# Optimization experiments

Measured on AMD Instinct MI355X. Metric: run time of the kernel, lower is better.

The kernel has to match this reference:

```python
import jax, jax.numpy as jnp
import numpy as np

N_NODES = 100000
N_EDGES = 1000000
NUM_GRAPHS = 500
EPS = 1e-5


def gcn_conv(x, src, dst, W, b, n_nodes):
    # PyG GCNConv: h = x @ W, symmetric norm with self-loops, aggregate at dst, add bias
    h = x @ W
    deg = jnp.zeros((n_nodes,), h.dtype).at[dst].add(1.0) + 1.0  # in-degree + self-loop
    dis = jax.lax.rsqrt(deg)
    msg = h[src] * (dis[src] * dis[dst])[:, None]               # [E, F] gather
    agg = jnp.zeros_like(h).at[dst].add(msg)                    # scatter-add
    return agg + h * (dis * dis)[:, None] + b                   # self-loop term + bias


def bn_eval(x, g, be, m, v):
    return (x - m) * jax.lax.rsqrt(v + EPS) * g + be


def setup_inputs() -> dict:
    key = jax.random.key(0)
    ks = jax.random.split(key, 8)
    edge_index = jax.random.randint(ks[0], (2, N_EDGES), 0, N_NODES, dtype=jnp.int32)
    batch = jnp.sort(jax.random.randint(ks[1], (N_NODES,), 0, NUM_GRAPHS, dtype=jnp.int32))
    d_in, h1, h2, hc, nc = 64, 64, 32, 16, 2
    return {
        "x": jax.random.normal(ks[2], (N_NODES, d_in), jnp.float32),
        "edge_index": edge_index,
        "batch": batch,
        "W1": jax.random.normal(ks[3], (d_in, h1), jnp.float32) / np.sqrt(d_in),
        "b1": jnp.zeros((h1,), jnp.float32),
        "g1": jnp.ones((h1,), jnp.float32),
        "be1": jnp.zeros((h1,), jnp.float32),
        "m1": jnp.zeros((h1,), jnp.float32),
        "v1": jnp.ones((h1,), jnp.float32),
        "W2": jax.random.normal(ks[4], (h1, h2), jnp.float32) / np.sqrt(h1),
        "b2": jnp.zeros((h2,), jnp.float32),
        "g2": jnp.ones((h2,), jnp.float32),
        "be2": jnp.zeros((h2,), jnp.float32),
        "m2": jnp.zeros((h2,), jnp.float32),
        "v2": jnp.ones((h2,), jnp.float32),
        "Wc1": jax.random.normal(ks[5], (h2, hc), jnp.float32) / np.sqrt(h2),
        "bc1": jnp.zeros((hc,), jnp.float32),
        "Wc2": jax.random.normal(ks[6], (hc, nc), jnp.float32) / np.sqrt(hc),
        "bc2": jnp.zeros((nc,), jnp.float32),
    }


def reference(x, edge_index, batch, W1, b1, g1, be1, m1, v1,
              W2, b2, g2, be2, m2, v2, Wc1, bc1, Wc2, bc2):
    src, dst = edge_index[0], edge_index[1]
    n = x.shape[0]
    # encoder layer 1: GCNConv -> BN(eval) -> ReLU  (dropout off in eval)
    h = jax.nn.relu(bn_eval(gcn_conv(x, src, dst, W1, b1, n), g1, be1, m1, v1))
    # encoder layer 2
    h = jax.nn.relu(bn_eval(gcn_conv(h, src, dst, W2, b2, n), g2, be2, m2, v2))
    # global mean pool over graphs
    sums = jax.ops.segment_sum(h, batch, num_segments=NUM_GRAPHS)
    cnts = jax.ops.segment_sum(jnp.ones((n,), h.dtype), batch, num_segments=NUM_GRAPHS)
    z = sums / jnp.maximum(cnts, 1.0)[:, None]                  # [NUM_GRAPHS, h2]
    # classifier MLP
    return jax.nn.relu(z @ Wc1 + bc1) @ Wc2 + bc2               # [NUM_GRAPHS, num_classes]
```

## Files before the change

kernel.cpp:

```cpp
#include <hip/hip_runtime.h>
#include <hip/hip_bf16.h>


#define CHUNK 4096

typedef float floatx2 __attribute__((ext_vector_type(2)));

__global__ void k_zero_misc(int* __restrict__ bucketCnt, float* __restrict__ sums,
                            int nSums) {
    int i = blockIdx.x * blockDim.x + threadIdx.x;
    if (i < 512) bucketCnt[i] = 0;
    int j = i - 512;
    if (j >= 0 && j < nSums) sums[j] = 0.f;
}

__global__ __launch_bounds__(256) void k_hist(const int* __restrict__ dst,
                                              int* __restrict__ bucketCnt, int E) {
    __shared__ int lh[512];
    for (int i = threadIdx.x; i < 512; i += 256) lh[i] = 0;
    __syncthreads();
    int base = blockIdx.x * CHUNK;
    for (int i = threadIdx.x; i < CHUNK; i += 256) {
        int e = base + i;
        if (e < E) atomicAdd(&lh[dst[e] >> 8], 1);
    }
    __syncthreads();
    for (int i = threadIdx.x; i < 512; i += 256)
        if (lh[i]) atomicAdd(&bucketCnt[i], lh[i]);
}

__global__ void k_scan512(const int* __restrict__ bucketCnt,
                          int* __restrict__ bucketStart,
                          int* __restrict__ bucketCursor) {
    __shared__ int s[512];
    int tid = threadIdx.x;
    int v = bucketCnt[tid];
    s[tid] = v;
    __syncthreads();
    for (int off = 1; off < 512; off <<= 1) {
        int t = (tid >= off) ? s[tid - off] : 0;
        __syncthreads();
        s[tid] += t;
        __syncthreads();
    }
    int excl = s[tid] - v;
    bucketStart[tid] = excl;
    bucketCursor[tid] = excl;
    if (tid == 511) bucketStart[512] = s[511];
}

__global__ __launch_bounds__(256) void k_binpairs(
    const int* __restrict__ src, const int* __restrict__ dst,
    int* __restrict__ bucketCursor, unsigned* __restrict__ pairs, int E) {
    __shared__ int lh[512];
    __shared__ int lbase[512];
    for (int i = threadIdx.x; i < 512; i += 256) lh[i] = 0;
    __syncthreads();
    int base = blockIdx.x * CHUNK;
    for (int i = threadIdx.x; i < CHUNK; i += 256) {
        int e = base + i;
        if (e < E) atomicAdd(&lh[dst[e] >> 8], 1);
    }
    __syncthreads();
    for (int i = threadIdx.x; i < 512; i += 256) {
        int c = lh[i];
        lbase[i] = c ? atomicAdd(&bucketCursor[i], c) : 0;
        lh[i] = 0;
    }
    __syncthreads();
    for (int i = threadIdx.x; i < CHUNK; i += 256) {
        int e = base + i;
        if (e < E) {
            int d = dst[e];
            int b = d >> 8;
            int r = atomicAdd(&lh[b], 1);
            pairs[lbase[b] + r] = ((unsigned)src[e] << 8) | (unsigned)(d & 255);
        }
    }
}

__global__ __launch_bounds__(256) void k_csr(
    const unsigned* __restrict__ pairs, const int* __restrict__ bucketStart,
    int* __restrict__ rowStart, float* __restrict__ dis, int* __restrict__ perm,
    int n, int E) {
    __shared__ int cnt[256];
    __shared__ int s[256];
    __shared__ int cur[256];
    int b = blockIdx.x, tid = threadIdx.x;
    int r0 = bucketStart[b], r1 = bucketStart[b + 1];
    cnt[tid] = 0;
    __syncthreads();
    for (int i = r0 + tid; i < r1; i += 256) atomicAdd(&cnt[pairs[i] & 255], 1);
    __syncthreads();
    int v = cnt[tid];
    s[tid] = v;
    __syncthreads();
    for (int off = 1; off < 256; off <<= 1) {
        int t = (tid >= off) ? s[tid - off] : 0;
        __syncthreads();
        s[tid] += t;
        __syncthreads();
    }
    int excl = s[tid] - v;
    int node = b * 256 + tid;
    if (node < n) {
        rowStart[node] = r0 + excl;
        dis[node] = rsqrtf((float)v + 1.0f);
    }
    if (b == 0 && tid == 0) rowStart[n] = E;
    cur[tid] = excl;
    __syncthreads();
    for (int i = r0 + tid; i < r1; i += 256) {
        unsigned p = pairs[i];
        int lo = p & 255;
        int slot = atomicAdd(&cur[lo], 1);
        perm[r0 + slot] = (int)(p >> 8);
    }
}

__global__ __launch_bounds__(256) void k_gemm64(
    const float* __restrict__ x, const float* __restrict__ W,
    const float* __restrict__ dis, unsigned char* __restrict__ hs8, int n) {
    __shared__ float Ws[64 * 64];
    __shared__ float xs[128][65];
    const int tid = threadIdx.x;
    for (int i = tid * 4; i < 4096; i += 1024)
        *(float4*)&Ws[i] = *(const float4*)&W[i];
    const int base = blockIdx.x * 128;
    for (int i = tid; i < 2048; i += 256) {
        int r = i >> 4;
        int k = (i & 15) * 4;
        int row = base + r;
        float4 xv = (row < n) ? *(const float4*)&x[(size_t)row * 64 + k]
                              : make_float4(0.f, 0.f, 0.f, 0.f);
        xs[r][k] = xv.x; xs[r][k + 1] = xv.y; xs[r][k + 2] = xv.z; xs[r][k + 3] = xv.w;
    }
    __syncthreads();
    const int cg = tid & 7;
    const int rg = tid >> 3;
    float acc[4][8] = {};
#pragma unroll 4
    for (int k = 0; k < 64; ++k) {
        float w8[8];
        *(float4*)&w8[0] = *(const float4*)&Ws[k * 64 + cg * 8];
        *(float4*)&w8[4] = *(const float4*)&Ws[k * 64 + cg * 8 + 4];
        float x4[4];
#pragma unroll
        for (int rr = 0; rr < 4; ++rr) x4[rr] = xs[rg * 4 + rr][k];
#pragma unroll
        for (int rr = 0; rr < 4; ++rr)
#pragma unroll
            for (int cc = 0; cc < 8; ++cc)
                acc[rr][cc] = fmaf(x4[rr], w8[cc], acc[rr][cc]);
    }
#pragma unroll
    for (int rr = 0; rr < 4; ++rr) {
        int row = base + rg * 4 + rr;
        if (row >= n) break;
        float d = dis[row];
        float v0 = acc[rr][0] * d, v1 = acc[rr][1] * d;
        float v2 = acc[rr][2] * d, v3 = acc[rr][3] * d;
        float v4 = acc[rr][4] * d, v5 = acc[rr][5] * d;
        float v6 = acc[rr][6] * d, v7 = acc[rr][7] * d;
        int q0 = __builtin_amdgcn_cvt_pk_fp8_f32(v0, v1, 0, false);
        q0 = __builtin_amdgcn_cvt_pk_fp8_f32(v2, v3, q0, true);
        int q1 = __builtin_amdgcn_cvt_pk_fp8_f32(v4, v5, 0, false);
        q1 = __builtin_amdgcn_cvt_pk_fp8_f32(v6, v7, q1, true);
        uint2 q = {(unsigned)q0, (unsigned)q1};
        *(uint2*)&hs8[(size_t)row * 64 + cg * 8] = q;
    }
}

__global__ __launch_bounds__(256) void k_gather64f8_gemm32(
    const unsigned char* __restrict__ hs8, const int* __restrict__ rowStart,
    const int* __restrict__ perm, const float* __restrict__ dis,
    const float* __restrict__ b, const float* __restrict__ g,
    const float* __restrict__ be, const float* __restrict__ m,
    const float* __restrict__ v, const float* __restrict__ W2,
    unsigned char* __restrict__ hs2f8, int n) {
    __shared__ float W2s[64 * 32];
    __shared__ float actS[16][68];
    for (int i = threadIdx.x * 4; i < 2048; i += 1024)
        *(float4*)&W2s[i] = *(const float4*)&W2[i];
    __syncthreads();

    const unsigned* hsu = (const unsigned*)hs8;
    int c = threadIdx.x & 15;
    int ln = threadIdx.x >> 4;
    int node = (blockIdx.x * 256 + threadIdx.x) >> 4;
    if (node >= n) return;
    int r0 = rowStart[node], r1 = rowStart[node + 1];
    float d = dis[node];
    float a0, a1, a2, a3;
    {
        unsigned su = hsu[(size_t)node * 16 + c];
        floatx2 lo = __builtin_amdgcn_cvt_pk_f32_fp8(su, false);
        floatx2 hi = __builtin_amdgcn_cvt_pk_f32_fp8(su, true);
        a0 = lo[0]; a1 = lo[1]; a2 = hi[0]; a3 = hi[1];
    }
    int e = r0;
    for (; e + 7 < r1; e += 8) {
        int s0 = perm[e],     s1 = perm[e + 1], s2 = perm[e + 2], s3 = perm[e + 3];
        int s4 = perm[e + 4], s5 = perm[e + 5], s6 = perm[e + 6], s7 = perm[e + 7];
        unsigned u0 = hsu[(size_t)s0 * 16 + c];
        unsigned u1 = hsu[(size_t)s1 * 16 + c];
        unsigned u2 = hsu[(size_t)s2 * 16 + c];
        unsigned u3 = hsu[(size_t)s3 * 16 + c];
        unsigned u4 = hsu[(size_t)s4 * 16 + c];
        unsigned u5 = hsu[(size_t)s5 * 16 + c];
        unsigned u6 = hsu[(size_t)s6 * 16 + c];
        unsigned u7 = hsu[(size_t)s7 * 16 + c];
#pragma unroll
        for (int j = 0; j < 8; ++j) {
            unsigned u = j == 0 ? u0 : j == 1 ? u1 : j == 2 ? u2 : j == 3 ? u3
                       : j == 4 ? u4 : j == 5 ? u5 : j == 6 ? u6 : u7;
            floatx2 lo = __builtin_amdgcn_cvt_pk_f32_fp8(u, false);
            floatx2 hi = __builtin_amdgcn_cvt_pk_f32_fp8(u, true);
            a0 += lo[0]; a1 += lo[1]; a2 += hi[0]; a3 += hi[1];
        }
    }
    for (; e < r1; ++e) {
        unsigned u = hsu[(size_t)perm[e] * 16 + c];
        floatx2 lo = __builtin_amdgcn_cvt_pk_f32_fp8(u, false);
        floatx2 hi = __builtin_amdgcn_cvt_pk_f32_fp8(u, true);
        a0 += lo[0]; a1 += lo[1]; a2 += hi[0]; a3 += hi[1];
    }
    int f = 4 * c;
    float4 gv = *(const float4*)&g[f];
    float4 vv = *(const float4*)&v[f];
    float4 bv = *(const float4*)&b[f];
    float4 mv = *(const float4*)&m[f];
    float4 bev = *(const float4*)&be[f];
    float sc0 = gv.x * rsqrtf(vv.x + 1e-5f), sc1 = gv.y * rsqrtf(vv.y + 1e-5f);
    float sc2 = gv.z * rsqrtf(vv.z + 1e-5f), sc3 = gv.w * rsqrtf(vv.w + 1e-5f);
    float y0 = fmaf(a0 * d, sc0, (bv.x - mv.x) * sc0 + bev.x);
    float y1 = fmaf(a1 * d, sc1, (bv.y - mv.y) * sc1 + bev.y);
    float y2 = fmaf(a2 * d, sc2, (bv.z - mv.z) * sc2 + bev.z);
    float y3 = fmaf(a3 * d, sc3, (bv.w - mv.w) * sc3 + bev.w);
    float4 yv = {y0 > 0.f ? y0 : 0.f, y1 > 0.f ? y1 : 0.f,
                 y2 > 0.f ? y2 : 0.f, y3 > 0.f ? y3 : 0.f};
    *(float4*)&actS[ln][f] = yv;

    float o0 = 0.f, o1 = 0.f;
#pragma unroll
    for (int k = 0; k < 64; ++k) {
        float a = actS[ln][k];
        o0 = fmaf(a, W2s[k * 32 + 2 * c], o0);
        o1 = fmaf(a, W2s[k * 32 + 2 * c + 1], o1);
    }
    int q = __builtin_amdgcn_cvt_pk_fp8_f32(o0 * d, o1 * d, 0, false);
    *(unsigned short*)&hs2f8[(size_t)node * 32 + 2 * c] = (unsigned short)q;
}

__global__ __launch_bounds__(256) void k_gather32f8(
    const unsigned char* __restrict__ hs8, const int* __restrict__ rowStart,
    const int* __restrict__ perm, const float* __restrict__ dis,
    const float* __restrict__ b, const float* __restrict__ g,
    const float* __restrict__ be, const float* __restrict__ m,
    const float* __restrict__ v, float* __restrict__ act, int n) {
    const unsigned* hsu = (const unsigned*)hs8;
    int c = threadIdx.x & 7;
    int node = (blockIdx.x * 256 + threadIdx.x) >> 3;
    if (node >= n) return;
    int r0 = rowStart[node], r1 = rowStart[node + 1];
    float d = dis[node];
    float a0, a1, a2, a3;
    {
        unsigned su = hsu[(size_t)node * 8 + c];
        floatx2 lo = __builtin_amdgcn_cvt_pk_f32_fp8(su, false);
        floatx2 hi = __builtin_amdgcn_cvt_pk_f32_fp8(su, true);
        a0 = lo[0]; a1 = lo[1]; a2 = hi[0]; a3 = hi[1];
    }
    int e = r0;
    for (; e + 7 < r1; e += 8) {
        int s0 = perm[e],     s1 = perm[e + 1], s2 = perm[e + 2], s3 = perm[e + 3];
        int s4 = perm[e + 4], s5 = perm[e + 5], s6 = perm[e + 6], s7 = perm[e + 7];
        unsigned u0 = hsu[(size_t)s0 * 8 + c];
        unsigned u1 = hsu[(size_t)s1 * 8 + c];
        unsigned u2 = hsu[(size_t)s2 * 8 + c];
        unsigned u3 = hsu[(size_t)s3 * 8 + c];
        unsigned u4 = hsu[(size_t)s4 * 8 + c];
        unsigned u5 = hsu[(size_t)s5 * 8 + c];
        unsigned u6 = hsu[(size_t)s6 * 8 + c];
        unsigned u7 = hsu[(size_t)s7 * 8 + c];
#pragma unroll
        for (int j = 0; j < 8; ++j) {
            unsigned u = j == 0 ? u0 : j == 1 ? u1 : j == 2 ? u2 : j == 3 ? u3
                       : j == 4 ? u4 : j == 5 ? u5 : j == 6 ? u6 : u7;
            floatx2 lo = __builtin_amdgcn_cvt_pk_f32_fp8(u, false);
            floatx2 hi = __builtin_amdgcn_cvt_pk_f32_fp8(u, true);
            a0 += lo[0]; a1 += lo[1]; a2 += hi[0]; a3 += hi[1];
        }
    }
    for (; e < r1; ++e) {
        unsigned u = hsu[(size_t)perm[e] * 8 + c];
        floatx2 lo = __builtin_amdgcn_cvt_pk_f32_fp8(u, false);
        floatx2 hi = __builtin_amdgcn_cvt_pk_f32_fp8(u, true);
        a0 += lo[0]; a1 += lo[1]; a2 += hi[0]; a3 += hi[1];
    }
    int f = 4 * c;
    float4 gv = *(const float4*)&g[f];
    float4 vv = *(const float4*)&v[f];
    float4 bv = *(const float4*)&b[f];
    float4 mv = *(const float4*)&m[f];
    float4 bev = *(const float4*)&be[f];
    float sc0 = gv.x * rsqrtf(vv.x + 1e-5f), sc1 = gv.y * rsqrtf(vv.y + 1e-5f);
    float sc2 = gv.z * rsqrtf(vv.z + 1e-5f), sc3 = gv.w * rsqrtf(vv.w + 1e-5f);
    float y0 = fmaf(a0 * d, sc0, (bv.x - mv.x) * sc0 + bev.x);
    float y1 = fmaf(a1 * d, sc1, (bv.y - mv.y) * sc1 + bev.y);
    float y2 = fmaf(a2 * d, sc2, (bv.z - mv.z) * sc2 + bev.z);
    float y3 = fmaf(a3 * d, sc3, (bv.w - mv.w) * sc3 + bev.w);
    float4 o = {y0 > 0.f ? y0 : 0.f, y1 > 0.f ? y1 : 0.f,
                y2 > 0.f ? y2 : 0.f, y3 > 0.f ? y3 : 0.f};
    *(float4*)&act[(size_t)node * 32 + f] = o;
}

__global__ __launch_bounds__(256) void k_pool(
    const float* __restrict__ act2, const int* __restrict__ batch,
    float* __restrict__ sums, float* __restrict__ cnt, int n) {
    int f = threadIdx.x & 31;
    int chunk = (blockIdx.x * blockDim.x + threadIdx.x) >> 5;
    int nchunks = (gridDim.x * blockDim.x) >> 5;
    int per = (n + nchunks - 1) / nchunks;
    int i0 = chunk * per;
    int i1 = min(n, i0 + per);
    if (i0 >= n) return;
    float acc = 0.f, c = 0.f;
    int cur = batch[i0];
    for (int i = i0; i < i1; ++i) {
        int bg = batch[i];
        if (bg != cur) {
            atomicAdd(&sums[(size_t)cur * 32 + f], acc);
            if (f == 0) atomicAdd(&cnt[cur], c);
            acc = 0.f; c = 0.f; cur = bg;
        }
        acc += act2[(size_t)i * 32 + f];
        c += 1.f;
    }
    atomicAdd(&sums[(size_t)cur * 32 + f], acc);
    if (f == 0) atomicAdd(&cnt[cur], c);
}

__global__ void k_mlp(const float* __restrict__ sums, const float* __restrict__ cnt,
                      const float* __restrict__ Wc1, const float* __restrict__ bc1,
                      const float* __restrict__ Wc2, const float* __restrict__ bc2,
                      float* __restrict__ out, int G) {
    int g = blockIdx.x * blockDim.x + threadIdx.x;
    if (g >= G) return;
    float c = cnt[g];
    c = c < 1.f ? 1.f : c;
    float inv = 1.f / c;
    float z[32];
#pragma unroll
    for (int j = 0; j < 32; ++j) z[j] = sums[(size_t)g * 32 + j] * inv;
    float o0 = bc2[0], o1 = bc2[1];
#pragma unroll
    for (int k = 0; k < 16; ++k) {
        float t = bc1[k];
#pragma unroll
        for (int j = 0; j < 32; ++j) t = fmaf(z[j], Wc1[j * 16 + k], t);
        t = t > 0.f ? t : 0.f;
        o0 = fmaf(t, Wc2[k * 2 + 0], o0);
        o1 = fmaf(t, Wc2[k * 2 + 1], o1);
    }
    out[g * 2 + 0] = o0;
    out[g * 2 + 1] = o1;
}

extern "C" void kernel_launch(void* const* d_in, const int* in_sizes, int n_in,
                              void* d_out, int out_size, void* d_ws, size_t ws_size,
                              hipStream_t stream) {
    const float* x   = (const float*)d_in[0];
    const int* ei    = (const int*)d_in[1];
    const int* batch = (const int*)d_in[2];
    const float* W1  = (const float*)d_in[3];
    const float* b1  = (const float*)d_in[4];
    const float* g1  = (const float*)d_in[5];
    const float* be1 = (const float*)d_in[6];
    const float* m1  = (const float*)d_in[7];
    const float* v1  = (const float*)d_in[8];
    const float* W2  = (const float*)d_in[9];
    const float* b2  = (const float*)d_in[10];
    const float* g2  = (const float*)d_in[11];
    const float* be2 = (const float*)d_in[12];
    const float* m2  = (const float*)d_in[13];
    const float* v2  = (const float*)d_in[14];
    const float* Wc1 = (const float*)d_in[15];
    const float* bc1 = (const float*)d_in[16];
    const float* Wc2 = (const float*)d_in[17];
    const float* bc2 = (const float*)d_in[18];

    const int n = in_sizes[2];
    const int E = in_sizes[1] / 2;
    const int G = out_size / 2;
    const int* srcI = ei;
    const int* dstI = ei + E;
    const int NB = (n + 255) >> 8;

    char* p = (char*)d_ws;
    auto alloc = [&](size_t bytes) {
        char* r = p;
        p += (bytes + 255) & ~(size_t)255;
        return r;
    };
    float*    dis          = (float*)alloc((size_t)n * 4);
    int*      bucketCnt    = (int*)alloc(512 * 4);
    int*      bucketStart  = (int*)alloc(513 * 4);
    int*      bucketCursor = (int*)alloc(512 * 4);
    unsigned* pairs        = (unsigned*)alloc((size_t)E * 4);
    int*      perm         = (int*)alloc((size_t)E * 4);
    int*      rowStart     = (int*)alloc(((size_t)n + 1) * 4);
    unsigned char* hs1f8   = (unsigned char*)alloc((size_t)64 * n);
    unsigned char* hs2f8   = (unsigned char*)alloc((size_t)32 * n);
    float*    act2         = (float*)alloc((size_t)32 * n * 4);
    float*    sums         = (float*)alloc((size_t)32 * G * 4 + (size_t)G * 4);
    float*    cntG         = sums + (size_t)32 * G;

    const int NT = 256;
    const int nbE = (E + CHUNK - 1) / CHUNK;
    const int nSums = G * 33;

    k_zero_misc<<<(512 + nSums + NT - 1) / NT, NT, 0, stream>>>(bucketCnt, sums, nSums);
    k_hist<<<nbE, NT, 0, stream>>>(dstI, bucketCnt, E);
    k_scan512<<<1, 512, 0, stream>>>(bucketCnt, bucketStart, bucketCursor);
    k_binpairs<<<nbE, NT, 0, stream>>>(srcI, dstI, bucketCursor, pairs, E);
    k_csr<<<NB, NT, 0, stream>>>(pairs, bucketStart, rowStart, dis, perm, n, E);

    k_gemm64<<<(n + 127) / 128, NT, 0, stream>>>(x, W1, dis, hs1f8, n);
    k_gather64f8_gemm32<<<(n * 16 + NT - 1) / NT, NT, 0, stream>>>(
        hs1f8, rowStart, perm, dis, b1, g1, be1, m1, v1, W2, hs2f8, n);

    k_gather32f8<<<(n * 8 + NT - 1) / NT, NT, 0, stream>>>(hs2f8, rowStart, perm, dis,
                                                           b2, g2, be2, m2, v2, act2, n);
    k_pool<<<1024, NT, 0, stream>>>(act2, batch, sums, cntG, n);

    k_mlp<<<(G + NT - 1) / NT, NT, 0, stream>>>(sums, cntG, Wc1, bc1, Wc2, bc2,
                                                (float*)d_out, G);
}
```

Before: 150.0 us.

## Fuse all stages into one persistent cooperative kernel with grid-wide syncs

Replaces the chain of ten kernel launches with one persistent cooperative kernel of 1024 blocks. Each stage runs as a grid-stride loop and stages are separated by grid.sync(), which removes per-launch overhead and tail gaps between launches. The cost is that every phase is limited to the co-resident grid, and the GEMM now reads W1 from global memory with 32-row tiles instead of a shared-memory-staged 128-row tile. It also adds serialized single-thread scans and grid barriers, and falls back to the old multi-kernel path if occupancy is too low.

```diff
diff --git a/kernel.cpp b/kernel.cpp
--- a/kernel.cpp
+++ b/kernel.cpp
@@ -1,10 +1,391 @@
 #include <hip/hip_runtime.h>
 #include <hip/hip_bf16.h>
+#include <hip/hip_cooperative_groups.h>
+
+namespace cg = cooperative_groups;
 
 
 #define CHUNK 4096
 
 typedef float floatx2 __attribute__((ext_vector_type(2)));
+
+struct Params {
+    const float* x; const int* src; const int* dst; const int* batch;
+    const float* W1; const float* b1; const float* g1; const float* be1;
+    const float* m1; const float* v1;
+    const float* W2; const float* b2; const float* g2; const float* be2;
+    const float* m2; const float* v2;
+    const float* Wc1; const float* bc1; const float* Wc2; const float* bc2;
+    float* out;
+    float* dis; int* bucketCnt; int* bucketStart; int* bucketCursor;
+    unsigned* pairs; int* perm; int* rowStart;
+    unsigned char* hs1f8; unsigned char* hs2f8; float* act2;
+    float* sums; float* cntG;
+    int n, E, G, NB;
+};
+
+union SMem {
+    struct { int lh[512]; int lbase[512]; } hist;
+    struct { int s[512]; } scan;
+    struct { int cnt[256]; int s[256]; int cur[256]; } csr;
+    struct { float xs[32][65]; } gemm;
+    struct { float W2s[64 * 32]; float actS[16][68]; } fg;
+};
+
+__global__ __launch_bounds__(256, 4) void k_mono(Params p) {
+    cg::grid_group grid = cg::this_grid();
+    __shared__ SMem sm;
+    const int tid = threadIdx.x;
+    const int bid = blockIdx.x;
+    const int nBlk = gridDim.x;
+
+    for (int i = bid * 256 + tid; i < 512 + p.G * 33; i += nBlk * 256) {
+        if (i < 512) p.bucketCnt[i] = 0;
+        else p.sums[i - 512] = 0.f;
+    }
+    grid.sync();
+
+    for (int cb = bid; cb * CHUNK < p.E; cb += nBlk) {
+        for (int i = tid; i < 512; i += 256) sm.hist.lh[i] = 0;
+        __syncthreads();
+        int base = cb * CHUNK;
+        for (int i = tid; i < CHUNK; i += 256) {
+            int e = base + i;
+            if (e < p.E) atomicAdd(&sm.hist.lh[p.dst[e] >> 8], 1);
+        }
+        __syncthreads();
+        for (int i = tid; i < 512; i += 256)
+            if (sm.hist.lh[i]) atomicAdd(&p.bucketCnt[i], sm.hist.lh[i]);
+        __syncthreads();
+    }
+    grid.sync();
+
+    if (bid == 0) {
+        for (int i = tid; i < 512; i += 256) sm.scan.s[i] = p.bucketCnt[i];
+        __syncthreads();
+        if (tid == 0) {
+            int acc = 0;
+            for (int i = 0; i < 512; ++i) {
+                int v = sm.scan.s[i];
+                sm.scan.s[i] = acc;
+                acc += v;
+            }
+        }
+        __syncthreads();
+        for (int i = tid; i < 512; i += 256) {
+            int e = sm.scan.s[i];
+            p.bucketStart[i] = e;
+            p.bucketCursor[i] = e;
+        }
+        if (tid == 0) p.bucketStart[512] = p.E;
+    }
+    grid.sync();
+
+    for (int cb = bid; cb * CHUNK < p.E; cb += nBlk) {
+        for (int i = tid; i < 512; i += 256) sm.hist.lh[i] = 0;
+        __syncthreads();
+        int base = cb * CHUNK;
+        for (int i = tid; i < CHUNK; i += 256) {
+            int e = base + i;
+            if (e < p.E) atomicAdd(&sm.hist.lh[p.dst[e] >> 8], 1);
+        }
+        __syncthreads();
+        for (int i = tid; i < 512; i += 256) {
+            int c = sm.hist.lh[i];
+            sm.hist.lbase[i] = c ? atomicAdd(&p.bucketCursor[i], c) : 0;
+            sm.hist.lh[i] = 0;
+        }
+        __syncthreads();
+        for (int i = tid; i < CHUNK; i += 256) {
+            int e = base + i;
+            if (e < p.E) {
+                int d = p.dst[e];
+                int b = d >> 8;
+                int r = atomicAdd(&sm.hist.lh[b], 1);
+                p.pairs[sm.hist.lbase[b] + r] =
+                    ((unsigned)p.src[e] << 8) | (unsigned)(d & 255);
+            }
+        }
+        __syncthreads();
+    }
+    grid.sync();
+
+    for (int b = bid; b < p.NB; b += nBlk) {
+        int r0 = p.bucketStart[b], r1 = p.bucketStart[b + 1];
+        sm.csr.cnt[tid] = 0;
+        __syncthreads();
+        for (int i = r0 + tid; i < r1; i += 256)
+            atomicAdd(&sm.csr.cnt[p.pairs[i] & 255], 1);
+        __syncthreads();
+        int v = sm.csr.cnt[tid];
+        sm.csr.s[tid] = v;
+        __syncthreads();
+        for (int off = 1; off < 256; off <<= 1) {
+            int t = (tid >= off) ? sm.csr.s[tid - off] : 0;
+            __syncthreads();
+            sm.csr.s[tid] += t;
+            __syncthreads();
+        }
+        int excl = sm.csr.s[tid] - v;
+        int node = b * 256 + tid;
+        if (node < p.n) {
+            p.rowStart[node] = r0 + excl;
+            p.dis[node] = rsqrtf((float)v + 1.0f);
+        }
+        if (b == 0 && tid == 0) p.rowStart[p.n] = p.E;
+        sm.csr.cur[tid] = excl;
+        __syncthreads();
+        for (int i = r0 + tid; i < r1; i += 256) {
+            unsigned pr = p.pairs[i];
+            int lo = pr & 255;
+            int slot = atomicAdd(&sm.csr.cur[lo], 1);
+            p.perm[r0 + slot] = (int)(pr >> 8);
+        }
+        __syncthreads();
+    }
+    grid.sync();
+
+    {
+        const int cg5 = tid & 7;
+        const int row5 = tid >> 3;
+        for (int t = bid; t * 32 < p.n; t += nBlk) {
+            __syncthreads();
+            int base = t * 32;
+            for (int i = tid; i < 512; i += 256) {
+                int r = i >> 4;
+                int k = (i & 15) * 4;
+                int row = base + r;
+                float4 xv = (row < p.n) ? *(const float4*)&p.x[(size_t)row * 64 + k]
+                                        : make_float4(0.f, 0.f, 0.f, 0.f);
+                sm.gemm.xs[r][k] = xv.x; sm.gemm.xs[r][k + 1] = xv.y;
+                sm.gemm.xs[r][k + 2] = xv.z; sm.gemm.xs[r][k + 3] = xv.w;
+            }
+            __syncthreads();
+            float acc[8] = {};
+#pragma unroll 4
+            for (int k = 0; k < 64; ++k) {
+                float4 wa = *(const float4*)&p.W1[k * 64 + cg5 * 8];
+                float4 wb = *(const float4*)&p.W1[k * 64 + cg5 * 8 + 4];
+                float xv = sm.gemm.xs[row5][k];
+                acc[0] = fmaf(xv, wa.x, acc[0]);
+                acc[1] = fmaf(xv, wa.y, acc[1]);
+                acc[2] = fmaf(xv, wa.z, acc[2]);
+                acc[3] = fmaf(xv, wa.w, acc[3]);
+                acc[4] = fmaf(xv, wb.x, acc[4]);
+                acc[5] = fmaf(xv, wb.y, acc[5]);
+                acc[6] = fmaf(xv, wb.z, acc[6]);
+                acc[7] = fmaf(xv, wb.w, acc[7]);
+            }
+            int row = base + row5;
+            if (row < p.n) {
+                float d = p.dis[row];
+                int q0 = __builtin_amdgcn_cvt_pk_fp8_f32(acc[0] * d, acc[1] * d, 0, false);
+                q0 = __builtin_amdgcn_cvt_pk_fp8_f32(acc[2] * d, acc[3] * d, q0, true);
+                int q1 = __builtin_amdgcn_cvt_pk_fp8_f32(acc[4] * d, acc[5] * d, 0, false);
+                q1 = __builtin_amdgcn_cvt_pk_fp8_f32(acc[6] * d, acc[7] * d, q1, true);
+                uint2 q = {(unsigned)q0, (unsigned)q1};
+                *(uint2*)&p.hs1f8[(size_t)row * 64 + cg5 * 8] = q;
+            }
+        }
+    }
+    grid.sync();
+
+    for (int i = tid * 4; i < 2048; i += 1024)
+        *(float4*)&sm.fg.W2s[i] = *(const float4*)&p.W2[i];
+    __syncthreads();
+    {
+        const unsigned* hsu = (const unsigned*)p.hs1f8;
+        int c = tid & 15;
+        int ln = tid >> 4;
+        int ngrp = (p.n + 15) >> 4;
+        for (int gp = bid; gp < ngrp; gp += nBlk) {
+            int node = gp * 16 + ln;
+            if (node < p.n) {
+                int r0 = p.rowStart[node], r1 = p.rowStart[node + 1];
+                float d = p.dis[node];
+                float a0, a1, a2, a3;
+                {
+                    unsigned su = hsu[(size_t)node * 16 + c];
+                    floatx2 lo = __builtin_amdgcn_cvt_pk_f32_fp8(su, false);
+                    floatx2 hi = __builtin_amdgcn_cvt_pk_f32_fp8(su, true);
+                    a0 = lo[0]; a1 = lo[1]; a2 = hi[0]; a3 = hi[1];
+                }
+                int e = r0;
+                for (; e + 7 < r1; e += 8) {
+                    int s0 = p.perm[e],     s1 = p.perm[e + 1];
+                    int s2 = p.perm[e + 2], s3 = p.perm[e + 3];
+                    int s4 = p.perm[e + 4], s5 = p.perm[e + 5];
+                    int s6 = p.perm[e + 6], s7 = p.perm[e + 7];
+                    unsigned u0 = hsu[(size_t)s0 * 16 + c];
+                    unsigned u1 = hsu[(size_t)s1 * 16 + c];
+                    unsigned u2 = hsu[(size_t)s2 * 16 + c];
+                    unsigned u3 = hsu[(size_t)s3 * 16 + c];
+                    unsigned u4 = hsu[(size_t)s4 * 16 + c];
+                    unsigned u5 = hsu[(size_t)s5 * 16 + c];
+                    unsigned u6 = hsu[(size_t)s6 * 16 + c];
+                    unsigned u7 = hsu[(size_t)s7 * 16 + c];
+#pragma unroll
+                    for (int j = 0; j < 8; ++j) {
+                        unsigned u = j == 0 ? u0 : j == 1 ? u1 : j == 2 ? u2 : j == 3 ? u3
+                                   : j == 4 ? u4 : j == 5 ? u5 : j == 6 ? u6 : u7;
+                        floatx2 lo = __builtin_amdgcn_cvt_pk_f32_fp8(u, false);
+                        floatx2 hi = __builtin_amdgcn_cvt_pk_f32_fp8(u, true);
+                        a0 += lo[0]; a1 += lo[1]; a2 += hi[0]; a3 += hi[1];
+                    }
+                }
+                for (; e < r1; ++e) {
+                    unsigned u = hsu[(size_t)p.perm[e] * 16 + c];
+                    floatx2 lo = __builtin_amdgcn_cvt_pk_f32_fp8(u, false);
+                    floatx2 hi = __builtin_amdgcn_cvt_pk_f32_fp8(u, true);
+                    a0 += lo[0]; a1 += lo[1]; a2 += hi[0]; a3 += hi[1];
+                }
+                int f = 4 * c;
+                float4 gv = *(const float4*)&p.g1[f];
+                float4 vv = *(const float4*)&p.v1[f];
+                float4 bv = *(const float4*)&p.b1[f];
+                float4 mv = *(const float4*)&p.m1[f];
+                float4 bev = *(const float4*)&p.be1[f];
+                float sc0 = gv.x * rsqrtf(vv.x + 1e-5f);
+                float sc1 = gv.y * rsqrtf(vv.y + 1e-5f);
+                float sc2 = gv.z * rsqrtf(vv.z + 1e-5f);
+                float sc3 = gv.w * rsqrtf(vv.w + 1e-5f);
+                float y0 = fmaf(a0 * d, sc0, (bv.x - mv.x) * sc0 + bev.x);
+                float y1 = fmaf(a1 * d, sc1, (bv.y - mv.y) * sc1 + bev.y);
+                float y2 = fmaf(a2 * d, sc2, (bv.z - mv.z) * sc2 + bev.z);
+                float y3 = fmaf(a3 * d, sc3, (bv.w - mv.w) * sc3 + bev.w);
+                float4 yv = {y0 > 0.f ? y0 : 0.f, y1 > 0.f ? y1 : 0.f,
+                             y2 > 0.f ? y2 : 0.f, y3 > 0.f ? y3 : 0.f};
+                *(float4*)&sm.fg.actS[ln][f] = yv;
+
+                float o0 = 0.f, o1 = 0.f;
+#pragma unroll
+                for (int k = 0; k < 64; ++k) {
+                    float a = sm.fg.actS[ln][k];
+                    o0 = fmaf(a, sm.fg.W2s[k * 32 + 2 * c], o0);
+                    o1 = fmaf(a, sm.fg.W2s[k * 32 + 2 * c + 1], o1);
+                }
+                int q = __builtin_amdgcn_cvt_pk_fp8_f32(o0 * d, o1 * d, 0, false);
+                *(unsigned short*)&p.hs2f8[(size_t)node * 32 + 2 * c] = (unsigned short)q;
+            }
+        }
+    }
+    grid.sync();
+
+    {
+        const unsigned* hsu = (const unsigned*)p.hs2f8;
+        int c = tid & 7;
+        int ngrp = (p.n + 31) >> 5;
+        for (int gp = bid; gp < ngrp; gp += nBlk) {
+            int node = gp * 32 + (tid >> 3);
+            if (node < p.n) {
+                int r0 = p.rowStart[node], r1 = p.rowStart[node + 1];
+                float d = p.dis[node];
+                float a0, a1, a2, a3;
+                {
+                    unsigned su = hsu[(size_t)node * 8 + c];
+                    floatx2 lo = __builtin_amdgcn_cvt_pk_f32_fp8(su, false);
+                    floatx2 hi = __builtin_amdgcn_cvt_pk_f32_fp8(su, true);
+                    a0 = lo[0]; a1 = lo[1]; a2 = hi[0]; a3 = hi[1];
+                }
+                int e = r0;
+                for (; e + 7 < r1; e += 8) {
+                    int s0 = p.perm[e],     s1 = p.perm[e + 1];
+                    int s2 = p.perm[e + 2], s3 = p.perm[e + 3];
+                    int s4 = p.perm[e + 4], s5 = p.perm[e + 5];
+                    int s6 = p.perm[e + 6], s7 = p.perm[e + 7];
+                    unsigned u0 = hsu[(size_t)s0 * 8 + c];
+                    unsigned u1 = hsu[(size_t)s1 * 8 + c];
+                    unsigned u2 = hsu[(size_t)s2 * 8 + c];
+                    unsigned u3 = hsu[(size_t)s3 * 8 + c];
+                    unsigned u4 = hsu[(size_t)s4 * 8 + c];
+                    unsigned u5 = hsu[(size_t)s5 * 8 + c];
+                    unsigned u6 = hsu[(size_t)s6 * 8 + c];
+                    unsigned u7 = hsu[(size_t)s7 * 8 + c];
+#pragma unroll
+                    for (int j = 0; j < 8; ++j) {
+                        unsigned u = j == 0 ? u0 : j == 1 ? u1 : j == 2 ? u2 : j == 3 ? u3
+                                   : j == 4 ? u4 : j == 5 ? u5 : j == 6 ? u6 : u7;
+                        floatx2 lo = __builtin_amdgcn_cvt_pk_f32_fp8(u, false);
+                        floatx2 hi = __builtin_amdgcn_cvt_pk_f32_fp8(u, true);
+                        a0 += lo[0]; a1 += lo[1]; a2 += hi[0]; a3 += hi[1];
+                    }
+                }
+                for (; e < r1; ++e) {
+                    unsigned u = hsu[(size_t)p.perm[e] * 8 + c];
+                    floatx2 lo = __builtin_amdgcn_cvt_pk_f32_fp8(u, false);
+                    floatx2 hi = __builtin_amdgcn_cvt_pk_f32_fp8(u, true);
+                    a0 += lo[0]; a1 += lo[1]; a2 += hi[0]; a3 += hi[1];
+                }
+                int f = 4 * c;
+                float4 gv = *(const float4*)&p.g2[f];
+                float4 vv = *(const float4*)&p.v2[f];
+                float4 bv = *(const float4*)&p.b2[f];
+                float4 mv = *(const float4*)&p.m2[f];
+                float4 bev = *(const float4*)&p.be2[f];
+                float sc0 = gv.x * rsqrtf(vv.x + 1e-5f);
+                float sc1 = gv.y * rsqrtf(vv.y + 1e-5f);
+                float sc2 = gv.z * rsqrtf(vv.z + 1e-5f);
+                float sc3 = gv.w * rsqrtf(vv.w + 1e-5f);
+                float y0 = fmaf(a0 * d, sc0, (bv.x - mv.x) * sc0 + bev.x);
+                float y1 = fmaf(a1 * d, sc1, (bv.y - mv.y) * sc1 + bev.y);
+                float y2 = fmaf(a2 * d, sc2, (bv.z - mv.z) * sc2 + bev.z);
+                float y3 = fmaf(a3 * d, sc3, (bv.w - mv.w) * sc3 + bev.w);
+                float4 o = {y0 > 0.f ? y0 : 0.f, y1 > 0.f ? y1 : 0.f,
+                            y2 > 0.f ? y2 : 0.f, y3 > 0.f ? y3 : 0.f};
+                *(float4*)&p.act2[(size_t)node * 32 + f] = o;
+            }
+        }
+    }
+    grid.sync();
+
+    {
+        int f = tid & 31;
+        int chunk = (bid * 256 + tid) >> 5;
+        int nchunks = (nBlk * 256) >> 5;
+        int per = (p.n + nchunks - 1) / nchunks;
+        int i0 = chunk * per;
+        int i1 = min(p.n, i0 + per);
+        if (i0 < p.n) {
+            float acc = 0.f, cn = 0.f;
+            int cur = p.batch[i0];
+            for (int i = i0; i < i1; ++i) {
+                int bg = p.batch[i];
+                if (bg != cur) {
+                    atomicAdd(&p.sums[(size_t)cur * 32 + f], acc);
+                    if (f == 0) atomicAdd(&p.cntG[cur], cn);
+                    acc = 0.f; cn = 0.f; cur = bg;
+                }
+                acc += p.act2[(size_t)i * 32 + f];
+                cn += 1.f;
+            }
+            atomicAdd(&p.sums[(size_t)cur * 32 + f], acc);
+            if (f == 0) atomicAdd(&p.cntG[cur], cn);
+        }
+    }
+    grid.sync();
+
+    for (int g = bid * 256 + tid; g < p.G; g += nBlk * 256) {
+        float cn = p.cntG[g];
+        cn = cn < 1.f ? 1.f : cn;
+        float inv = 1.f / cn;
+        float z[32];
+#pragma unroll
+        for (int j = 0; j < 32; ++j) z[j] = p.sums[(size_t)g * 32 + j] * inv;
+        float o0 = p.bc2[0], o1 = p.bc2[1];
+#pragma unroll
+        for (int k = 0; k < 16; ++k) {
+            float t = p.bc1[k];
+#pragma unroll
+            for (int j = 0; j < 32; ++j) t = fmaf(z[j], p.Wc1[j * 16 + k], t);
+            t = t > 0.f ? t : 0.f;
+            o0 = fmaf(t, p.Wc2[k * 2 + 0], o0);
+            o1 = fmaf(t, p.Wc2[k * 2 + 1], o1);
+        }
+        p.out[g * 2 + 0] = o0;
+        p.out[g * 2 + 1] = o1;
+    }
+}
+
 
 __global__ void k_zero_misc(int* __restrict__ bucketCnt, float* __restrict__ sums,
                             int nSums) {
@@ -111,10 +492,10 @@
     cur[tid] = excl;
     __syncthreads();
     for (int i = r0 + tid; i < r1; i += 256) {
-        unsigned p = pairs[i];
-        int lo = p & 255;
+        unsigned pr = pairs[i];
+        int lo = pr & 255;
         int slot = atomicAdd(&cur[lo], 1);
-        perm[r0 + slot] = (int)(p >> 8);
+        perm[r0 + slot] = (int)(pr >> 8);
     }
 }
 
@@ -158,14 +539,10 @@
         int row = base + rg * 4 + rr;
         if (row >= n) break;
         float d = dis[row];
-        float v0 = acc[rr][0] * d, v1 = acc[rr][1] * d;
-        float v2 = acc[rr][2] * d, v3 = acc[rr][3] * d;
-        float v4 = acc[rr][4] * d, v5 = acc[rr][5] * d;
-        float v6 = acc[rr][6] * d, v7 = acc[rr][7] * d;
-        int q0 = __builtin_amdgcn_cvt_pk_fp8_f32(v0, v1, 0, false);
-        q0 = __builtin_amdgcn_cvt_pk_fp8_f32(v2, v3, q0, true);
-        int q1 = __builtin_amdgcn_cvt_pk_fp8_f32(v4, v5, 0, false);
-        q1 = __builtin_amdgcn_cvt_pk_fp8_f32(v6, v7, q1, true);
+        int q0 = __builtin_amdgcn_cvt_pk_fp8_f32(acc[rr][0] * d, acc[rr][1] * d, 0, false);
+        q0 = __builtin_amdgcn_cvt_pk_fp8_f32(acc[rr][2] * d, acc[rr][3] * d, q0, true);
+        int q1 = __builtin_amdgcn_cvt_pk_fp8_f32(acc[rr][4] * d, acc[rr][5] * d, 0, false);
+        q1 = __builtin_amdgcn_cvt_pk_fp8_f32(acc[rr][6] * d, acc[rr][7] * d, q1, true);
         uint2 q = {(unsigned)q0, (unsigned)q1};
         *(uint2*)&hs8[(size_t)row * 64 + cg * 8] = q;
     }
@@ -183,7 +560,6 @@
     for (int i = threadIdx.x * 4; i < 2048; i += 1024)
         *(float4*)&W2s[i] = *(const float4*)&W2[i];
     __syncthreads();
-
     const unsigned* hsu = (const unsigned*)hs8;
     int c = threadIdx.x & 15;
     int ln = threadIdx.x >> 4;
@@ -240,7 +616,6 @@
     float4 yv = {y0 > 0.f ? y0 : 0.f, y1 > 0.f ? y1 : 0.f,
                  y2 > 0.f ? y2 : 0.f, y3 > 0.f ? y3 : 0.f};
     *(float4*)&actS[ln][f] = yv;
-
     float o0 = 0.f, o1 = 0.f;
 #pragma unroll
     for (int k = 0; k < 64; ++k) {
@@ -370,70 +745,74 @@
 extern "C" void kernel_launch(void* const* d_in, const int* in_sizes, int n_in,
                               void* d_out, int out_size, void* d_ws, size_t ws_size,
                               hipStream_t stream) {
-    const float* x   = (const float*)d_in[0];
-    const int* ei    = (const int*)d_in[1];
-    const int* batch = (const int*)d_in[2];
-    const float* W1  = (const float*)d_in[3];
-    const float* b1  = (const float*)d_in[4];
-    const float* g1  = (const float*)d_in[5];
-    const float* be1 = (const float*)d_in[6];
-    const float* m1  = (const float*)d_in[7];
-    const float* v1  = (const float*)d_in[8];
-    const float* W2  = (const float*)d_in[9];
-    const float* b2  = (const float*)d_in[10];
-    const float* g2  = (const float*)d_in[11];
-    const float* be2 = (const float*)d_in[12];
-    const float* m2  = (const float*)d_in[13];
-    const float* v2  = (const float*)d_in[14];
-    const float* Wc1 = (const float*)d_in[15];
-    const float* bc1 = (const float*)d_in[16];
-    const float* Wc2 = (const float*)d_in[17];
-    const float* bc2 = (const float*)d_in[18];
-
     const int n = in_sizes[2];
     const int E = in_sizes[1] / 2;
     const int G = out_size / 2;
-    const int* srcI = ei;
-    const int* dstI = ei + E;
-    const int NB = (n + 255) >> 8;
-
-    char* p = (char*)d_ws;
+
+    char* pw = (char*)d_ws;
     auto alloc = [&](size_t bytes) {
-        char* r = p;
-        p += (bytes + 255) & ~(size_t)255;
+        char* r = pw;
+        pw += (bytes + 255) & ~(size_t)255;
         return r;
     };
-    float*    dis          = (float*)alloc((size_t)n * 4);
-    int*      bucketCnt    = (int*)alloc(512 * 4);
-    int*      bucketStart  = (int*)alloc(513 * 4);
-    int*      bucketCursor = (int*)alloc(512 * 4);
-    unsigned* pairs        = (unsigned*)alloc((size_t)E * 4);
-    int*      perm         = (int*)alloc((size_t)E * 4);
-    int*      rowStart     = (int*)alloc(((size_t)n + 1) * 4);
-    unsigned char* hs1f8   = (unsigned char*)alloc((size_t)64 * n);
-    unsigned char* hs2f8   = (unsigned char*)alloc((size_t)32 * n);
-    float*    act2         = (float*)alloc((size_t)32 * n * 4);
-    float*    sums         = (float*)alloc((size_t)32 * G * 4 + (size_t)G * 4);
-    float*    cntG         = sums + (size_t)32 * G;
+
+    Params p;
+    p.x   = (const float*)d_in[0];
+    p.src = (const int*)d_in[1];
+    p.dst = ((const int*)d_in[1]) + E;
+    p.batch = (const int*)d_in[2];
+    p.W1 = (const float*)d_in[3];  p.b1 = (const float*)d_in[4];
+    p.g1 = (const float*)d_in[5];  p.be1 = (const float*)d_in[6];
+    p.m1 = (const float*)d_in[7];  p.v1 = (const float*)d_in[8];
+    p.W2 = (const float*)d_in[9];  p.b2 = (const float*)d_in[10];
+    p.g2 = (const float*)d_in[11]; p.be2 = (const float*)d_in[12];
+    p.m2 = (const float*)d_in[13]; p.v2 = (const float*)d_in[14];
+    p.Wc1 = (const float*)d_in[15]; p.bc1 = (const float*)d_in[16];
+    p.Wc2 = (const float*)d_in[17]; p.bc2 = (const float*)d_in[18];
+    p.out = (float*)d_out;
+
+    p.dis          = (float*)alloc((size_t)n * 4);
+    p.bucketCnt    = (int*)alloc(512 * 4);
+    p.bucketStart  = (int*)alloc(513 * 4);
+    p.bucketCursor = (int*)alloc(512 * 4);
+    p.pairs        = (unsigned*)alloc((size_t)E * 4);
+    p.perm         = (int*)alloc((size_t)E * 4);
+    p.rowStart     = (int*)alloc(((size_t)n + 1) * 4);
+    p.hs1f8        = (unsigned char*)alloc((size_t)64 * n);
+    p.hs2f8        = (unsigned char*)alloc((size_t)32 * n);
+    p.act2         = (float*)alloc((size_t)32 * n * 4);
+    p.sums         = (float*)alloc((size_t)32 * G * 4 + (size_t)G * 4);
+    p.cntG         = p.sums + (size_t)32 * G;
+
+    p.n = n; p.E = E; p.G = G;
+    p.NB = (n + 255) >> 8;
+
+    int bpcu = 0;
+    hipError_t oe = hipOccupancyMaxActiveBlocksPerMultiprocessor(&bpcu, k_mono, 256, 0);
+    bool done = false;
+    if (oe == hipSuccess && bpcu >= 4) {
+        void* args[] = { &p };
+        hipError_t le = hipLaunchCooperativeKernel((void*)k_mono, dim3(1024),
+                                                   dim3(256), args, 0, stream);
+        done = (le == hipSuccess);
+    }
+    if (done) return;
 
     const int NT = 256;
     const int nbE = (E + CHUNK - 1) / CHUNK;
     const int nSums = G * 33;
 
-    k_zero_misc<<<(512 + nSums + NT - 1) / NT, NT, 0, stream>>>(bucketCnt, sums, nSums);
-    k_hist<<<nbE, NT, 0, stream>>>(dstI, bucketCnt, E);
-    k_scan512<<<1, 512, 0, stream>>>(bucketCnt, bucketStart, bucketCursor);
-    k_binpairs<<<nbE, NT, 0, stream>>>(srcI, dstI, bucketCursor, pairs, E);
-    k_csr<<<NB, NT, 0, stream>>>(pairs, bucketStart, rowStart, dis, perm, n, E);
-
-    k_gemm64<<<(n + 127) / 128, NT, 0, stream>>>(x, W1, dis, hs1f8, n);
+    k_zero_misc<<<(512 + nSums + NT - 1) / NT, NT, 0, stream>>>(p.bucketCnt, p.sums, nSums);
+    k_hist<<<nbE, NT, 0, stream>>>(p.dst, p.bucketCnt, E);
+    k_scan512<<<1, 512, 0, stream>>>(p.bucketCnt, p.bucketStart, p.bucketCursor);
+    k_binpairs<<<nbE, NT, 0, stream>>>(p.src, p.dst, p.bucketCursor, p.pairs, E);
+    k_csr<<<p.NB, NT, 0, stream>>>(p.pairs, p.bucketStart, p.rowStart, p.dis, p.perm, n, E);
+    k_gemm64<<<(n + 127) / 128, NT, 0, stream>>>(p.x, p.W1, p.dis, p.hs1f8, n);
     k_gather64f8_gemm32<<<(n * 16 + NT - 1) / NT, NT, 0, stream>>>(
-        hs1f8, rowStart, perm, dis, b1, g1, be1, m1, v1, W2, hs2f8, n);
-
-    k_gather32f8<<<(n * 8 + NT - 1) / NT, NT, 0, stream>>>(hs2f8, rowStart, perm, dis,
-                                                           b2, g2, be2, m2, v2, act2, n);
-    k_pool<<<1024, NT, 0, stream>>>(act2, batch, sums, cntG, n);
-
-    k_mlp<<<(G + NT - 1) / NT, NT, 0, stream>>>(sums, cntG, Wc1, bc1, Wc2, bc2,
-                                                (float*)d_out, G);
-}
+        p.hs1f8, p.rowStart, p.perm, p.dis, p.b1, p.g1, p.be1, p.m1, p.v1, p.W2, p.hs2f8, n);
+    k_gather32f8<<<(n * 8 + NT - 1) / NT, NT, 0, stream>>>(
+        p.hs2f8, p.rowStart, p.perm, p.dis, p.b2, p.g2, p.be2, p.m2, p.v2, p.act2, n);
+    k_pool<<<1024, NT, 0, stream>>>(p.act2, p.batch, p.sums, p.cntG, n);
+    k_mlp<<<(G + NT - 1) / NT, NT, 0, stream>>>(p.sums, p.cntG, p.Wc1, p.bc1,
+                                                p.Wc2, p.bc2, p.out, G);
+}
```

Result: no change. 150.4 us (+0.2%).
